# Performance work log

Measured on AMD Instinct MI355X. Metric: run time of the kernel, lower is better.

Reference implementation:

```python
import jax, jax.numpy as jnp
import numpy as np

N, C, H, W = 8, 256, 64, 64
Q_REDUCE, K_REDUCE, V_REDUCE = 8, 8, 1


def setup_inputs() -> dict:
    key = jax.random.key(0)
    ks = jax.random.split(key, 6)
    Cq, Ck, Cv = C // Q_REDUCE, C // K_REDUCE, C // V_REDUCE
    s = 0.02
    x = jax.random.normal(ks[0], (N, C, H, W), dtype=jnp.float32)
    Wq = jax.random.normal(ks[1], (Cq, C), dtype=jnp.float32) * s
    Wk = jax.random.normal(ks[2], (Ck, C), dtype=jnp.float32) * s
    Wv = jax.random.normal(ks[3], (Cv, C), dtype=jnp.float32) * s
    Wo = jax.random.normal(ks[4], (C, Cv), dtype=jnp.float32) * s
    gamma = jax.random.normal(ks[5], (), dtype=jnp.float32)  # trained scalar (init 0.0 in torch)
    return {"x": x, "Wq": Wq, "Wk": Wk, "Wv": Wv, "Wo": Wo, "gamma": gamma}


def reference(x, Wq, Wk, Wv, Wo, gamma):
    n, c, h, w = x.shape
    xf = x.reshape(n, c, h * w)                      # [N, C, HW]
    q = jnp.einsum('qc,ncl->nql', Wq, xf)            # [N, Cq, HW] (1x1 conv)
    k = jnp.einsum('kc,ncl->nkl', Wk, xf)            # [N, Ck, HW]
    v = jnp.einsum('vc,ncl->nvl', Wv, xf)            # [N, Cv, HW]
    e = jnp.einsum('nci,ncj->nij', q, k)             # [N, HW, HW], unscaled energies
    a = jax.nn.softmax(e, axis=-1)                   # softmax over keys j
    o = jnp.einsum('nvi,nij->nvj', v, a)             # [N, Cv, HW]  (o = bmm(v, a))
    o = o.reshape(n, -1, w, h)                       # faithful: view(N,-1,W,H)
    out = jnp.einsum('ov,nvhw->nohw', Wo, o)         # output 1x1 conv
    return gamma * out
```

## Files before the change

### kernel.cpp

```cpp
#include <hip/hip_runtime.h>
#include <hip/hip_bf16.h>

#define NB 8
#define CIN 256
#define LL 4096
#define CQ 32
#define CV 256

typedef __attribute__((ext_vector_type(8))) short bf16x8;
typedef __attribute__((ext_vector_type(4))) float f32x4;

__device__ __forceinline__ unsigned short f2bf(float f) {
    union { __hip_bfloat16 h; unsigned short u; } c;
    c.h = __float2bfloat16(f);
    return c.u;
}
__device__ __forceinline__ float bf2f(unsigned short h) {
    return __uint_as_float(((unsigned)h) << 16);
}

__device__ __forceinline__ void barrier_lds_only() {
    asm volatile("s_waitcnt lgkmcnt(0)" ::: "memory");
    __builtin_amdgcn_s_barrier();
}

__global__ __launch_bounds__(256) void k_wcast(
    const float* __restrict__ Wq, const float* __restrict__ Wk,
    const float* __restrict__ Wv, const float* __restrict__ Wo,
    unsigned short* __restrict__ Wb, unsigned short* __restrict__ Wob)
{
    const float LOG2E = 1.4426950408889634f;
    const int row = blockIdx.x, t = threadIdx.x;
    if (row < 320) {
        float val;
        if (row < 32)      val = Wq[row * 256 + t] * LOG2E;
        else if (row < 64) val = Wk[(row - 32) * 256 + t];
        else               val = Wv[(row - 64) * 256 + t];
        Wb[row * 256 + t] = f2bf(val);
    } else {
        const int r2 = row - 320;
        Wob[r2 * 256 + t] = f2bf(Wo[r2 * 256 + t]);
    }
}

__global__ __launch_bounds__(512) void k_qkv3(
    const float* __restrict__ x, const unsigned short* __restrict__ Wb,
    unsigned short* __restrict__ qkt, unsigned short* __restrict__ v)
{
    __shared__ unsigned short xlds[64][264];
    __shared__ unsigned short tr[64][72];
    const int n = blockIdx.y, l0 = blockIdx.x * 64, t = threadIdx.x;
    const int w = t >> 6, lane = t & 63, lid = lane & 15, quad = lane >> 4;

    #pragma unroll
    for (int part = 0; part < 4; part++) {
        const int cbase = part * 64 + w * 8;
        float tmp[8];
        #pragma unroll
        for (int cc = 0; cc < 8; cc++)
            tmp[cc] = x[((size_t)n * CIN + cbase + cc) * LL + l0 + lane];
        bf16x8 s;
        #pragma unroll
        for (int cc = 0; cc < 8; cc++) s[cc] = (short)f2bf(tmp[cc]);
        *(bf16x8*)&xlds[lane][cbase] = s;
    }
    __syncthreads();

    const f32x4 fzero = {0.f, 0.f, 0.f, 0.f};
    f32x4 acc[3][4];
    #pragma unroll
    for (int mt = 0; mt < 3; mt++)
        #pragma unroll
        for (int nt = 0; nt < 4; nt++) acc[mt][nt] = fzero;

    for (int k0 = 0; k0 < 256; k0 += 32) {
        bf16x8 bx[4];
        #pragma unroll
        for (int nt = 0; nt < 4; nt++)
            bx[nt] = *(const bf16x8*)&xlds[nt * 16 + lid][k0 + quad * 8];
        #pragma unroll
        for (int vt = 0; vt < 2; vt++) {
            const bf16x8 wa = *(const bf16x8*)&Wb[(64 + w * 32 + vt * 16 + lid) * 256 + k0 + quad * 8];
            #pragma unroll
            for (int nt = 0; nt < 4; nt++)
                acc[vt][nt] = __builtin_amdgcn_mfma_f32_16x16x32_bf16(wa, bx[nt], acc[vt][nt], 0, 0, 0);
        }
        if (w < 4) {
            const bf16x8 wa = *(const bf16x8*)&Wb[(w * 16 + lid) * 256 + k0 + quad * 8];
            #pragma unroll
            for (int nt = 0; nt < 4; nt++)
                acc[2][nt] = __builtin_amdgcn_mfma_f32_16x16x32_bf16(wa, bx[nt], acc[2][nt], 0, 0, 0);
        }
    }
    #pragma unroll
    for (int vt = 0; vt < 2; vt++)
        #pragma unroll
        for (int nt = 0; nt < 4; nt++)
            #pragma unroll
            for (int reg = 0; reg < 4; reg++) {
                const int vr = w * 32 + vt * 16 + quad * 4 + reg;
                v[((size_t)n * CV + vr) * LL + l0 + nt * 16 + lid] = f2bf(acc[vt][nt][reg]);
            }
    if (w < 4) {
        #pragma unroll
        for (int nt = 0; nt < 4; nt++)
            #pragma unroll
            for (int reg = 0; reg < 4; reg++)
                tr[nt * 16 + lid][w * 16 + quad * 4 + reg] = f2bf(acc[2][nt][reg]);
    }
    __syncthreads();
    {
        const int l = t >> 3, c = (t & 7) * 8;
        *(uint4*)&qkt[((size_t)n * LL + l0 + l) * 64 + c] = *(const uint4*)&tr[l][c];
    }
}

__global__ __launch_bounds__(512) void k_rowsum3(
    const unsigned short* __restrict__ qkt, float* __restrict__ lns)
{
    __shared__ float red[64];
    const int n = blockIdx.y, i0 = blockIdx.x * 64, t = threadIdx.x;
    const int w = t >> 6, lid = t & 15, quad = (t & 63) >> 4;
    if (t < 64) red[t] = 0.f;
    __syncthreads();

    bf16x8 aq[4];
    #pragma unroll
    for (int mt = 0; mt < 4; mt++)
        aq[mt] = *(const bf16x8*)&qkt[((size_t)n * LL + i0 + mt * 16 + lid) * 64 + quad * 8];

    const f32x4 fzero = {0.f, 0.f, 0.f, 0.f};
    float sums[4][4];
    #pragma unroll
    for (int mt = 0; mt < 4; mt++)
        #pragma unroll
        for (int reg = 0; reg < 4; reg++) sums[mt][reg] = 0.f;

    for (int jt = 0; jt < 8; jt++) {
        const int j0 = jt * 512 + w * 64;
        bf16x8 bk[4];
        #pragma unroll
        for (int nt = 0; nt < 4; nt++)
            bk[nt] = *(const bf16x8*)&qkt[((size_t)n * LL + j0 + nt * 16 + lid) * 64 + 32 + quad * 8];
        #pragma unroll
        for (int mt = 0; mt < 4; mt++)
            #pragma unroll
            for (int nt = 0; nt < 4; nt++) {
                f32x4 e = __builtin_amdgcn_mfma_f32_16x16x32_bf16(aq[mt], bk[nt], fzero, 0, 0, 0);
                sums[mt][0] += __builtin_amdgcn_exp2f(e[0]);
                sums[mt][1] += __builtin_amdgcn_exp2f(e[1]);
                sums[mt][2] += __builtin_amdgcn_exp2f(e[2]);
                sums[mt][3] += __builtin_amdgcn_exp2f(e[3]);
            }
    }
    #pragma unroll
    for (int mt = 0; mt < 4; mt++)
        #pragma unroll
        for (int reg = 0; reg < 4; reg++) {
            float s = sums[mt][reg];
            s += __shfl_xor(s, 1); s += __shfl_xor(s, 2);
            s += __shfl_xor(s, 4); s += __shfl_xor(s, 8);
            if (lid == 0) atomicAdd(&red[mt * 16 + quad * 4 + reg], s);
        }
    __syncthreads();
    if (t < 64) lns[(size_t)n * LL + i0 + t] = -__builtin_log2f(red[t]);
}

__global__ __launch_bounds__(512, 4) void k_attn12(
    const unsigned short* __restrict__ qkt, const unsigned short* __restrict__ v,
    const float* __restrict__ lns, const unsigned short* __restrict__ Wob,
    const float* __restrict__ gp, float* __restrict__ out)
{
    __shared__ unsigned short pbuf[2][4][4][64][8];
    __shared__ unsigned short olds[64][264];

    const int bid = blockIdx.x;
    const int n = bid & 7, j0 = (bid >> 3) * 64, t = threadIdx.x;
    const int w = t >> 6, lane = t & 63, lid = lane & 15, quad = lane >> 4;
    const int kbw = w >> 1;
    const int qr = (w & 1) * 2 + (quad >> 1);
    const int e0 = (quad & 1) * 4;

    const unsigned short* qrow = qkt + ((size_t)n * LL + w * 16 + lid) * 64 + quad * 8;
    const float* lrow = lns + (size_t)n * LL + w * 16 + quad * 4;
    const unsigned short* vrow = v + ((size_t)n * CV + w * 32 + lid) * LL + quad * 8;

    bf16x8 bk[4];
    #pragma unroll
    for (int nt = 0; nt < 4; nt++)
        bk[nt] = *(const bf16x8*)&qkt[((size_t)n * LL + j0 + nt * 16 + lid) * 64 + 32 + quad * 8];

    const f32x4 fzero = {0.f, 0.f, 0.f, 0.f};
    f32x4 acc[2][4];
    #pragma unroll
    for (int mt = 0; mt < 2; mt++)
        #pragma unroll
        for (int nt = 0; nt < 4; nt++) acc[mt][nt] = fzero;

    bf16x8 aq = *(const bf16x8*)qrow;
    f32x4 lnsC = *(const f32x4*)lrow;
    {
        f32x4 e[4];
        #pragma unroll
        for (int nt = 0; nt < 4; nt++)
            e[nt] = __builtin_amdgcn_mfma_f32_16x16x32_bf16(aq, bk[nt], lnsC, 0, 0, 0);
        aq = *(const bf16x8*)(qrow + (size_t)128 * 64);
        lnsC = *(const f32x4*)(lrow + 128);
        #pragma unroll
        for (int nt = 0; nt < 4; nt++) {
            ushort4 s;
            s.x = f2bf(__builtin_amdgcn_exp2f(e[nt][0]));
            s.y = f2bf(__builtin_amdgcn_exp2f(e[nt][1]));
            s.z = f2bf(__builtin_amdgcn_exp2f(e[nt][2]));
            s.w = f2bf(__builtin_amdgcn_exp2f(e[nt][3]));
            *(ushort4*)&pbuf[0][nt][kbw][qr * 16 + lid][e0] = s;
        }
    }
    bf16x8 av[8];
    #pragma unroll
    for (int mt = 0; mt < 2; mt++)
        #pragma unroll
        for (int h = 0; h < 4; h++)
            av[mt * 4 + h] = *(const bf16x8*)(vrow + (size_t)mt * 16 * LL + h * 32);
    barrier_lds_only();

    for (int ic = 0; ic < 31; ic++) {
        const int cur = ic & 1;
        const size_t i0 = (size_t)ic * 128;
        f32x4 e2[4];
        __builtin_amdgcn_s_setprio(1);
        #pragma unroll
        for (int nt = 0; nt < 4; nt++)
            e2[nt] = __builtin_amdgcn_mfma_f32_16x16x32_bf16(aq, bk[nt], lnsC, 0, 0, 0);
        __builtin_amdgcn_s_setprio(0);
        const size_t ipf = (ic < 30) ? (i0 + 256) : i0;
        aq = *(const bf16x8*)(qrow + ipf * 64);
        lnsC = *(const f32x4*)(lrow + ipf);
        #pragma unroll
        for (int nt = 0; nt < 4; nt++) {
            ushort4 s;
            s.x = f2bf(__builtin_amdgcn_exp2f(e2[nt][0]));
            s.y = f2bf(__builtin_amdgcn_exp2f(e2[nt][1]));
            s.z = f2bf(__builtin_amdgcn_exp2f(e2[nt][2]));
            s.w = f2bf(__builtin_amdgcn_exp2f(e2[nt][3]));
            *(ushort4*)&pbuf[cur ^ 1][nt][kbw][qr * 16 + lid][e0] = s;
        }
        #pragma unroll
        for (int h = 0; h < 4; h++) {
            bf16x8 bp[4];
            #pragma unroll
            for (int nt = 0; nt < 4; nt++)
                bp[nt] = *(const bf16x8*)&pbuf[cur][nt][h][lane][0];
            __builtin_amdgcn_s_setprio(1);
            #pragma unroll
            for (int mt = 0; mt < 2; mt++)
                #pragma unroll
                for (int nt = 0; nt < 4; nt++)
                    acc[mt][nt] = __builtin_amdgcn_mfma_f32_16x16x32_bf16(av[mt * 4 + h], bp[nt], acc[mt][nt], 0, 0, 0);
            __builtin_amdgcn_s_setprio(0);
            #pragma unroll
            for (int mt = 0; mt < 2; mt++)
                av[mt * 4 + h] = *(const bf16x8*)(vrow + (size_t)mt * 16 * LL + (i0 + 128) + h * 32);
        }
        barrier_lds_only();
    }
    #pragma unroll
    for (int h = 0; h < 4; h++) {
        bf16x8 bp[4];
        #pragma unroll
        for (int nt = 0; nt < 4; nt++)
            bp[nt] = *(const bf16x8*)&pbuf[1][nt][h][lane][0];
        __builtin_amdgcn_s_setprio(1);
        #pragma unroll
        for (int mt = 0; mt < 2; mt++)
            #pragma unroll
            for (int nt = 0; nt < 4; nt++)
                acc[mt][nt] = __builtin_amdgcn_mfma_f32_16x16x32_bf16(av[mt * 4 + h], bp[nt], acc[mt][nt], 0, 0, 0);
        __builtin_amdgcn_s_setprio(0);
    }
    __syncthreads();

    #pragma unroll
    for (int mt = 0; mt < 2; mt++)
        #pragma unroll
        for (int nt = 0; nt < 4; nt++) {
            ushort4 s;
            s.x = f2bf(acc[mt][nt][0]); s.y = f2bf(acc[mt][nt][1]);
            s.z = f2bf(acc[mt][nt][2]); s.w = f2bf(acc[mt][nt][3]);
            *(ushort4*)&olds[nt * 16 + lid][w * 32 + mt * 16 + quad * 4] = s;
        }
    __syncthreads();
    f32x4 oacc[2][4];
    #pragma unroll
    for (int mt = 0; mt < 2; mt++)
        #pragma unroll
        for (int nt = 0; nt < 4; nt++) oacc[mt][nt] = fzero;
    for (int k0 = 0; k0 < 256; k0 += 32) {
        bf16x8 bo[4];
        #pragma unroll
        for (int nt = 0; nt < 4; nt++)
            bo[nt] = *(const bf16x8*)&olds[nt * 16 + lid][k0 + quad * 8];
        #pragma unroll
        for (int mt = 0; mt < 2; mt++) {
            const bf16x8 wa = *(const bf16x8*)&Wob[(w * 32 + mt * 16 + lid) * 256 + k0 + quad * 8];
            #pragma unroll
            for (int nt = 0; nt < 4; nt++)
                oacc[mt][nt] = __builtin_amdgcn_mfma_f32_16x16x32_bf16(wa, bo[nt], oacc[mt][nt], 0, 0, 0);
        }
    }
    const float g = *gp;
    #pragma unroll
    for (int mt = 0; mt < 2; mt++)
        #pragma unroll
        for (int nt = 0; nt < 4; nt++)
            #pragma unroll
            for (int reg = 0; reg < 4; reg++) {
                const int r = w * 32 + mt * 16 + quad * 4 + reg;
                out[((size_t)n * CIN + r) * LL + j0 + nt * 16 + lid] = g * oacc[mt][nt][reg];
            }
}

extern "C" void kernel_launch(void* const* d_in, const int* in_sizes, int n_in,
                              void* d_out, int out_size, void* d_ws, size_t ws_size,
                              hipStream_t stream) {
    const float* x     = (const float*)d_in[0];
    const float* Wq    = (const float*)d_in[1];
    const float* Wk    = (const float*)d_in[2];
    const float* Wv    = (const float*)d_in[3];
    const float* Wo    = (const float*)d_in[4];
    const float* gamma = (const float*)d_in[5];

    unsigned short* qkt = (unsigned short*)d_ws;
    unsigned short* v   = qkt + (size_t)NB * LL * 64;
    unsigned short* Wb  = v + (size_t)NB * CV * LL;
    unsigned short* Wob = Wb + 320 * 256;
    float* lns          = (float*)(Wob + 256 * 256);
    float* out = (float*)d_out;

    k_wcast  <<<dim3(576),   256, 0, stream>>>(Wq, Wk, Wv, Wo, Wb, Wob);
    k_qkv3   <<<dim3(64, 8), 512, 0, stream>>>(x, Wb, qkt, v);
    k_rowsum3<<<dim3(64, 8), 512, 0, stream>>>(qkt, lns);
    k_attn12 <<<dim3(512),   512, 0, stream>>>(qkt, v, lns, Wob, gamma, out);
}
```

Before: 264.6 us.

## Warp-specialize attention kernel into softmax producer and PV consumer waves

The attention kernel grows from 512 to 1024 threads per block. Waves 0-7 compute the QK energies and exp into the double-buffered LDS P tile, and waves 8-15 load V and run the PV MFMAs. The two groups stay in step through the existing per-chunk barriers, and the output projection is split across all 16 waves. The aim is to overlap exp/convert work with the PV matrix math. The cost is twice the threads per block, which may reduce occupancy under the launch-bounds (1024, 4) request and raises register pressure.

```diff
diff --git a/kernel.cpp b/kernel.cpp
--- a/kernel.cpp
+++ b/kernel.cpp
@@ -166,7 +166,7 @@
     if (t < 64) lns[(size_t)n * LL + i0 + t] = -__builtin_log2f(red[t]);
 }
 
-__global__ __launch_bounds__(512, 4) void k_attn12(
+__global__ __launch_bounds__(1024, 4) void k_attn14(
     const unsigned short* __restrict__ qkt, const unsigned short* __restrict__ v,
     const float* __restrict__ lns, const unsigned short* __restrict__ Wob,
     const float* __restrict__ gp, float* __restrict__ out)
@@ -176,81 +176,110 @@
 
     const int bid = blockIdx.x;
     const int n = bid & 7, j0 = (bid >> 3) * 64, t = threadIdx.x;
-    const int w = t >> 6, lane = t & 63, lid = lane & 15, quad = lane >> 4;
-    const int kbw = w >> 1;
-    const int qr = (w & 1) * 2 + (quad >> 1);
-    const int e0 = (quad & 1) * 4;
-
-    const unsigned short* qrow = qkt + ((size_t)n * LL + w * 16 + lid) * 64 + quad * 8;
-    const float* lrow = lns + (size_t)n * LL + w * 16 + quad * 4;
-    const unsigned short* vrow = v + ((size_t)n * CV + w * 32 + lid) * LL + quad * 8;
-
-    bf16x8 bk[4];
-    #pragma unroll
-    for (int nt = 0; nt < 4; nt++)
-        bk[nt] = *(const bf16x8*)&qkt[((size_t)n * LL + j0 + nt * 16 + lid) * 64 + 32 + quad * 8];
-
+    const int w16 = t >> 6, lane = t & 63, lid = lane & 15, quad = lane >> 4;
     const f32x4 fzero = {0.f, 0.f, 0.f, 0.f};
+
     f32x4 acc[2][4];
     #pragma unroll
     for (int mt = 0; mt < 2; mt++)
         #pragma unroll
         for (int nt = 0; nt < 4; nt++) acc[mt][nt] = fzero;
 
-    bf16x8 aq = *(const bf16x8*)qrow;
-    f32x4 lnsC = *(const f32x4*)lrow;
-    {
-        f32x4 e[4];
-        #pragma unroll
-        for (int nt = 0; nt < 4; nt++)
-            e[nt] = __builtin_amdgcn_mfma_f32_16x16x32_bf16(aq, bk[nt], lnsC, 0, 0, 0);
-        aq = *(const bf16x8*)(qrow + (size_t)128 * 64);
-        lnsC = *(const f32x4*)(lrow + 128);
-        #pragma unroll
-        for (int nt = 0; nt < 4; nt++) {
-            ushort4 s;
-            s.x = f2bf(__builtin_amdgcn_exp2f(e[nt][0]));
-            s.y = f2bf(__builtin_amdgcn_exp2f(e[nt][1]));
-            s.z = f2bf(__builtin_amdgcn_exp2f(e[nt][2]));
-            s.w = f2bf(__builtin_amdgcn_exp2f(e[nt][3]));
-            *(ushort4*)&pbuf[0][nt][kbw][qr * 16 + lid][e0] = s;
-        }
-    }
-    bf16x8 av[8];
-    #pragma unroll
-    for (int mt = 0; mt < 2; mt++)
-        #pragma unroll
-        for (int h = 0; h < 4; h++)
-            av[mt * 4 + h] = *(const bf16x8*)(vrow + (size_t)mt * 16 * LL + h * 32);
-    barrier_lds_only();
-
-    for (int ic = 0; ic < 31; ic++) {
-        const int cur = ic & 1;
-        const size_t i0 = (size_t)ic * 128;
-        f32x4 e2[4];
-        __builtin_amdgcn_s_setprio(1);
-        #pragma unroll
-        for (int nt = 0; nt < 4; nt++)
-            e2[nt] = __builtin_amdgcn_mfma_f32_16x16x32_bf16(aq, bk[nt], lnsC, 0, 0, 0);
-        __builtin_amdgcn_s_setprio(0);
-        const size_t ipf = (ic < 30) ? (i0 + 256) : i0;
-        aq = *(const bf16x8*)(qrow + ipf * 64);
-        lnsC = *(const f32x4*)(lrow + ipf);
-        #pragma unroll
-        for (int nt = 0; nt < 4; nt++) {
-            ushort4 s;
-            s.x = f2bf(__builtin_amdgcn_exp2f(e2[nt][0]));
-            s.y = f2bf(__builtin_amdgcn_exp2f(e2[nt][1]));
-            s.z = f2bf(__builtin_amdgcn_exp2f(e2[nt][2]));
-            s.w = f2bf(__builtin_amdgcn_exp2f(e2[nt][3]));
-            *(ushort4*)&pbuf[cur ^ 1][nt][kbw][qr * 16 + lid][e0] = s;
+    if (w16 < 8) {
+        const int w = w16;
+        const int kbw = w >> 1;
+        const int qr = (w & 1) * 2 + (quad >> 1);
+        const int e0 = (quad & 1) * 4;
+        const unsigned short* qrow = qkt + ((size_t)n * LL + w * 16 + lid) * 64 + quad * 8;
+        const float* lrow = lns + (size_t)n * LL + w * 16 + quad * 4;
+
+        bf16x8 bk[4];
+        #pragma unroll
+        for (int nt = 0; nt < 4; nt++)
+            bk[nt] = *(const bf16x8*)&qkt[((size_t)n * LL + j0 + nt * 16 + lid) * 64 + 32 + quad * 8];
+
+        bf16x8 aq = *(const bf16x8*)qrow;
+        f32x4 lnsC = *(const f32x4*)lrow;
+        {
+            f32x4 e[4];
+            #pragma unroll
+            for (int nt = 0; nt < 4; nt++)
+                e[nt] = __builtin_amdgcn_mfma_f32_16x16x32_bf16(aq, bk[nt], lnsC, 0, 0, 0);
+            aq = *(const bf16x8*)(qrow + (size_t)128 * 64);
+            lnsC = *(const f32x4*)(lrow + 128);
+            #pragma unroll
+            for (int nt = 0; nt < 4; nt++) {
+                ushort4 s;
+                s.x = f2bf(__builtin_amdgcn_exp2f(e[nt][0]));
+                s.y = f2bf(__builtin_amdgcn_exp2f(e[nt][1]));
+                s.z = f2bf(__builtin_amdgcn_exp2f(e[nt][2]));
+                s.w = f2bf(__builtin_amdgcn_exp2f(e[nt][3]));
+                *(ushort4*)&pbuf[0][nt][kbw][qr * 16 + lid][e0] = s;
+            }
+        }
+        barrier_lds_only();
+
+        for (int ic = 0; ic < 31; ic++) {
+            const int cur = ic & 1;
+            const size_t i0 = (size_t)ic * 128;
+            f32x4 e2[4];
+            #pragma unroll
+            for (int nt = 0; nt < 4; nt++)
+                e2[nt] = __builtin_amdgcn_mfma_f32_16x16x32_bf16(aq, bk[nt], lnsC, 0, 0, 0);
+            const size_t ipf = (ic < 30) ? (i0 + 256) : i0;
+            aq = *(const bf16x8*)(qrow + ipf * 64);
+            lnsC = *(const f32x4*)(lrow + ipf);
+            #pragma unroll
+            for (int nt = 0; nt < 4; nt++) {
+                ushort4 s;
+                s.x = f2bf(__builtin_amdgcn_exp2f(e2[nt][0]));
+                s.y = f2bf(__builtin_amdgcn_exp2f(e2[nt][1]));
+                s.z = f2bf(__builtin_amdgcn_exp2f(e2[nt][2]));
+                s.w = f2bf(__builtin_amdgcn_exp2f(e2[nt][3]));
+                *(ushort4*)&pbuf[cur ^ 1][nt][kbw][qr * 16 + lid][e0] = s;
+            }
+            barrier_lds_only();
+        }
+    } else {
+        const int c = w16 - 8;
+        const unsigned short* vrow = v + ((size_t)n * CV + c * 32 + lid) * LL + quad * 8;
+
+        bf16x8 av[8];
+        #pragma unroll
+        for (int mt = 0; mt < 2; mt++)
+            #pragma unroll
+            for (int h = 0; h < 4; h++)
+                av[mt * 4 + h] = *(const bf16x8*)(vrow + (size_t)mt * 16 * LL + h * 32);
+        barrier_lds_only();
+
+        for (int ic = 0; ic < 31; ic++) {
+            const int cur = ic & 1;
+            const size_t i0 = (size_t)ic * 128;
+            #pragma unroll
+            for (int h = 0; h < 4; h++) {
+                bf16x8 bp[4];
+                #pragma unroll
+                for (int nt = 0; nt < 4; nt++)
+                    bp[nt] = *(const bf16x8*)&pbuf[cur][nt][h][lane][0];
+                __builtin_amdgcn_s_setprio(1);
+                #pragma unroll
+                for (int mt = 0; mt < 2; mt++)
+                    #pragma unroll
+                    for (int nt = 0; nt < 4; nt++)
+                        acc[mt][nt] = __builtin_amdgcn_mfma_f32_16x16x32_bf16(av[mt * 4 + h], bp[nt], acc[mt][nt], 0, 0, 0);
+                __builtin_amdgcn_s_setprio(0);
+                #pragma unroll
+                for (int mt = 0; mt < 2; mt++)
+                    av[mt * 4 + h] = *(const bf16x8*)(vrow + (size_t)mt * 16 * LL + (i0 + 128) + h * 32);
+            }
+            barrier_lds_only();
         }
         #pragma unroll
         for (int h = 0; h < 4; h++) {
             bf16x8 bp[4];
             #pragma unroll
             for (int nt = 0; nt < 4; nt++)
-                bp[nt] = *(const bf16x8*)&pbuf[cur][nt][h][lane][0];
+                bp[nt] = *(const bf16x8*)&pbuf[1][nt][h][lane][0];
             __builtin_amdgcn_s_setprio(1);
             #pragma unroll
             for (int mt = 0; mt < 2; mt++)
@@ -258,66 +287,40 @@
                 for (int nt = 0; nt < 4; nt++)
                     acc[mt][nt] = __builtin_amdgcn_mfma_f32_16x16x32_bf16(av[mt * 4 + h], bp[nt], acc[mt][nt], 0, 0, 0);
             __builtin_amdgcn_s_setprio(0);
-            #pragma unroll
-            for (int mt = 0; mt < 2; mt++)
-                av[mt * 4 + h] = *(const bf16x8*)(vrow + (size_t)mt * 16 * LL + (i0 + 128) + h * 32);
-        }
-        barrier_lds_only();
-    }
-    #pragma unroll
-    for (int h = 0; h < 4; h++) {
-        bf16x8 bp[4];
-        #pragma unroll
-        for (int nt = 0; nt < 4; nt++)
-            bp[nt] = *(const bf16x8*)&pbuf[1][nt][h][lane][0];
-        __builtin_amdgcn_s_setprio(1);
+        }
         #pragma unroll
         for (int mt = 0; mt < 2; mt++)
             #pragma unroll
-            for (int nt = 0; nt < 4; nt++)
-                acc[mt][nt] = __builtin_amdgcn_mfma_f32_16x16x32_bf16(av[mt * 4 + h], bp[nt], acc[mt][nt], 0, 0, 0);
-        __builtin_amdgcn_s_setprio(0);
-    }
-    __syncthreads();
-
-    #pragma unroll
-    for (int mt = 0; mt < 2; mt++)
-        #pragma unroll
-        for (int nt = 0; nt < 4; nt++) {
-            ushort4 s;
-            s.x = f2bf(acc[mt][nt][0]); s.y = f2bf(acc[mt][nt][1]);
-            s.z = f2bf(acc[mt][nt][2]); s.w = f2bf(acc[mt][nt][3]);
-            *(ushort4*)&olds[nt * 16 + lid][w * 32 + mt * 16 + quad * 4] = s;
-        }
-    __syncthreads();
-    f32x4 oacc[2][4];
-    #pragma unroll
-    for (int mt = 0; mt < 2; mt++)
-        #pragma unroll
-        for (int nt = 0; nt < 4; nt++) oacc[mt][nt] = fzero;
+            for (int nt = 0; nt < 4; nt++) {
+                ushort4 s;
+                s.x = f2bf(acc[mt][nt][0]); s.y = f2bf(acc[mt][nt][1]);
+                s.z = f2bf(acc[mt][nt][2]); s.w = f2bf(acc[mt][nt][3]);
+                *(ushort4*)&olds[nt * 16 + lid][c * 32 + mt * 16 + quad * 4] = s;
+            }
+    }
+    __syncthreads();
+
+    f32x4 oacc[4];
+    #pragma unroll
+    for (int nt = 0; nt < 4; nt++) oacc[nt] = fzero;
     for (int k0 = 0; k0 < 256; k0 += 32) {
         bf16x8 bo[4];
         #pragma unroll
         for (int nt = 0; nt < 4; nt++)
             bo[nt] = *(const bf16x8*)&olds[nt * 16 + lid][k0 + quad * 8];
-        #pragma unroll
-        for (int mt = 0; mt < 2; mt++) {
-            const bf16x8 wa = *(const bf16x8*)&Wob[(w * 32 + mt * 16 + lid) * 256 + k0 + quad * 8];
-            #pragma unroll
-            for (int nt = 0; nt < 4; nt++)
-                oacc[mt][nt] = __builtin_amdgcn_mfma_f32_16x16x32_bf16(wa, bo[nt], oacc[mt][nt], 0, 0, 0);
-        }
+        const bf16x8 wa = *(const bf16x8*)&Wob[(w16 * 16 + lid) * 256 + k0 + quad * 8];
+        #pragma unroll
+        for (int nt = 0; nt < 4; nt++)
+            oacc[nt] = __builtin_amdgcn_mfma_f32_16x16x32_bf16(wa, bo[nt], oacc[nt], 0, 0, 0);
     }
     const float g = *gp;
     #pragma unroll
-    for (int mt = 0; mt < 2; mt++)
-        #pragma unroll
-        for (int nt = 0; nt < 4; nt++)
-            #pragma unroll
-            for (int reg = 0; reg < 4; reg++) {
-                const int r = w * 32 + mt * 16 + quad * 4 + reg;
-                out[((size_t)n * CIN + r) * LL + j0 + nt * 16 + lid] = g * oacc[mt][nt][reg];
-            }
+    for (int nt = 0; nt < 4; nt++)
+        #pragma unroll
+        for (int reg = 0; reg < 4; reg++) {
+            const int r = w16 * 16 + quad * 4 + reg;
+            out[((size_t)n * CIN + r) * LL + j0 + nt * 16 + lid] = g * oacc[nt][reg];
+        }
 }
 
 extern "C" void kernel_launch(void* const* d_in, const int* in_sizes, int n_in,
@@ -340,5 +343,5 @@
     k_wcast  <<<dim3(576),   256, 0, stream>>>(Wq, Wk, Wv, Wo, Wb, Wob);
     k_qkv3   <<<dim3(64, 8), 512, 0, stream>>>(x, Wb, qkt, v);
     k_rowsum3<<<dim3(64, 8), 512, 0, stream>>>(qkt, lns);
-    k_attn12 <<<dim3(512),   512, 0, stream>>>(qkt, v, lns, Wob, gamma, out);
-}
+    k_attn14 <<<dim3(512),  1024, 0, stream>>>(qkt, v, lns, Wob, gamma, out);
+}
```

Result: no change. 265.6 us (+0.4%).
